# Kernel optimization log

Hardware: AMD Instinct MI355X
Metric: run time of the kernel (lower is better)

The kernel has to match this reference:

```python
import jax, jax.numpy as jnp
import numpy as np
from jax import lax

NUM_QUBITS = 4
NUM_LAYERS = 2
EPS = 1e-5  # BatchNorm eps; eval mode with running_mean=0, running_var=1


def _cnot_ring_matrix():
    # CNOT(0,1); CNOT(1,2); CNOT(2,3); CNOT(3,0) as one 16x16 permutation.
    # PennyLane convention: wire 0 is the most-significant bit of the basis index.
    M = np.zeros((16, 16), dtype=np.complex64)
    for b in range(16):
        bb = b
        for cw, tw in [(0, 1), (1, 2), (2, 3), (3, 0)]:
            if (bb >> (3 - cw)) & 1:
                bb ^= 1 << (3 - tw)
        M[bb, b] = 1.0
    return M

CNOT_RING = jnp.asarray(_cnot_ring_matrix())
# ZSIGNS[w, b] = <b|Z_w|b> = +/-1
ZSIGNS = jnp.asarray(np.array([[1.0 - 2.0 * ((b >> (3 - w)) & 1) for b in range(16)]
                               for w in range(NUM_QUBITS)], dtype=np.float32))


def conv_bn_relu(x, w, b, gamma, beta):
    # Conv2d(k=3, pad=1) + BatchNorm2d (eval: mean=0, var=1) + ReLU, NCHW
    x = lax.conv_general_dilated(x, w, (1, 1), ((1, 1), (1, 1)),
                                 dimension_numbers=('NCHW', 'OIHW', 'NCHW'))
    x = x + b[None, :, None, None]
    x = gamma[None, :, None, None] * x * (1.0 / np.sqrt(1.0 + EPS)) + beta[None, :, None, None]
    return jax.nn.relu(x)


def maxpool2(x):
    return lax.reduce_window(x, -jnp.inf, lax.max, (1, 1, 2, 2), (1, 1, 2, 2), 'VALID')


def avgpool2(x):
    return lax.reduce_window(x, 0.0, lax.add, (1, 1, 2, 2), (1, 1, 2, 2), 'VALID') * 0.25


def quantum_layer(x, weights):
    # x: [B, 16] softmax outputs. Amplitude-encode (abs + L2 normalize), then
    # BasicEntanglerLayers (RX rotations + CNOT ring) x NUM_LAYERS, then <Z_i>.
    psi = jnp.abs(x)
    psi = psi / jnp.linalg.norm(psi, axis=1, keepdims=True)
    psi = psi.astype(jnp.complex64)  # [B, 16] batched statevectors
    for l in range(NUM_LAYERS):
        c = jnp.cos(weights[l] * 0.5).astype(jnp.complex64)
        s = jnp.sin(weights[l] * 0.5).astype(jnp.complex64)
        U = jnp.ones((1, 1), dtype=jnp.complex64)
        for q in range(NUM_QUBITS):
            g = jnp.stack([jnp.stack([c[q], -1j * s[q]]),
                           jnp.stack([-1j * s[q], c[q]])])  # RX(theta_q)
            U = jnp.kron(U, g)
        U = CNOT_RING @ U  # rotations first, then entangling ring
        psi = psi @ U.T    # batched apply: [B,16] x [16,16]
    probs = jnp.real(psi * jnp.conj(psi))  # [B, 16]
    return probs @ ZSIGNS.T                # [B, 4] Pauli-Z expvals


def setup_inputs() -> dict:
    key = jax.random.key(0)
    ks = jax.random.split(key, 16)
    B = 1024
    f32 = jnp.float32

    def w(k, shape, fan_in):
        return jax.random.normal(k, shape, dtype=f32) * np.float32(1.0 / np.sqrt(fan_in))

    inp = {
        'x': jax.random.normal(ks[0], (B, 3, 32, 32), dtype=f32),
        'conv1_w': w(ks[1], (32, 3, 3, 3), 3 * 9), 'conv1_b': jnp.zeros((32,), f32),
        'bn1_g': jnp.ones((32,), f32), 'bn1_b': jnp.zeros((32,), f32),
        'conv2_w': w(ks[2], (64, 32, 3, 3), 32 * 9), 'conv2_b': jnp.zeros((64,), f32),
        'bn2_g': jnp.ones((64,), f32), 'bn2_b': jnp.zeros((64,), f32),
        'conv3_w': w(ks[3], (128, 64, 3, 3), 64 * 9), 'conv3_b': jnp.zeros((128,), f32),
        'bn3_g': jnp.ones((128,), f32), 'bn3_b': jnp.zeros((128,), f32),
        'fr1_w': w(ks[4], (512, 2048), 2048), 'fr1_b': jnp.zeros((512,), f32),
        'fr2_w': w(ks[5], (16, 512), 512), 'fr2_b': jnp.zeros((16,), f32),
        'q_weights': jax.random.uniform(ks[6], (NUM_LAYERS, NUM_QUBITS), dtype=f32,
                                        minval=0.0, maxval=2.0 * np.pi),
        'h1_w': w(ks[7], (128, 4), 4), 'h1_b': jnp.zeros((128,), f32),
        'bnh_g': jnp.ones((128,), f32), 'bnh_b': jnp.zeros((128,), f32),
        'h2_w': w(ks[8], (100, 128), 128), 'h2_b': jnp.zeros((100,), f32),
    }
    return inp


def reference(x, conv1_w, conv1_b, bn1_g, bn1_b, conv2_w, conv2_b, bn2_g, bn2_b,
              conv3_w, conv3_b, bn3_g, bn3_b, fr1_w, fr1_b, fr2_w, fr2_b,
              q_weights, h1_w, h1_b, bnh_g, bnh_b, h2_w, h2_b):
    # classical_net (CIFAR100 branch)
    h = conv_bn_relu(x, conv1_w, conv1_b, bn1_g, bn1_b)
    h = maxpool2(h)                                   # [B,32,16,16]
    h = conv_bn_relu(h, conv2_w, conv2_b, bn2_g, bn2_b)
    h = maxpool2(h)                                   # [B,64,8,8]
    h = conv_bn_relu(h, conv3_w, conv3_b, bn3_g, bn3_b)  # [B,128,8,8]
    h = avgpool2(h)                                   # AdaptiveAvgPool2d((4,4)): 8->4
    h = h.reshape(h.shape[0], -1)                     # [B, 2048]
    # feature_reducer
    h = jax.nn.relu(h @ fr1_w.T + fr1_b)
    f = jax.nn.softmax(h @ fr2_w.T + fr2_b, axis=1)   # [B, 16]
    # quantum layer (batched 4-qubit statevector sim)
    q = quantum_layer(f, q_weights)                   # [B, 4]
    # head (BN eval-mode, Dropout inactive)
    y = q @ h1_w.T + h1_b
    y = bnh_g * y * (1.0 / np.sqrt(1.0 + EPS)) + bnh_b
    y = jax.nn.relu(y)
    return y @ h2_w.T + h2_b                          # [B, 100]
```

## Files before the change

### kernel.cpp

```cpp
#include <hip/hip_runtime.h>
#include <math.h>

#define NB 1024
static constexpr float BN_INV = 0.99999500003749975f;

typedef __attribute__((ext_vector_type(8))) short short8;
typedef __attribute__((ext_vector_type(4))) float f32x4;

__device__ inline short f2bf(float f) {
  union { float f; unsigned u; } v;
  v.f = f;
  unsigned u = v.u;
  u += 0x7fff + ((u >> 16) & 1);
  return (short)(u >> 16);
}

__global__ void k_prepack(const float* __restrict__ c2w, const float* __restrict__ c2b,
                          const float* __restrict__ g2, const float* __restrict__ be2,
                          const float* __restrict__ c3w, const float* __restrict__ c3b,
                          const float* __restrict__ g3, const float* __restrict__ be3,
                          const float* __restrict__ fr1w,
                          short* __restrict__ wp2, short* __restrict__ wp3,
                          float* __restrict__ scsh, short* __restrict__ wfr1) {
  int i = blockIdx.x * 256 + threadIdx.x;
  int stride = gridDim.x * 256;
  for (int e = i; e < 18432; e += stride) {
    int j = e & 7, lane = (e >> 3) & 63, ct = (e >> 9) & 3, off = e >> 11;
    int co = ct * 16 + (lane & 15), ci = (lane >> 4) * 8 + j;
    wp2[e] = f2bf(c2w[(co * 32 + ci) * 9 + off]);
  }
  for (int e = i; e < 73728; e += stride) {
    int j = e & 7, lane = (e >> 3) & 63, ct = (e >> 9) & 7, oh = e >> 12;
    int half = oh & 1, off = oh >> 1;
    int co = ct * 16 + (lane & 15), ci = half * 32 + (lane >> 4) * 8 + j;
    wp3[e] = f2bf(c3w[(co * 64 + ci) * 9 + off]);
  }
  for (int e = i; e < 524288; e += stride) {
    float2 f = ((const float2*)fr1w)[e];
    unsigned lo = (unsigned)(unsigned short)f2bf(f.x);
    unsigned hi = (unsigned)(unsigned short)f2bf(f.y);
    ((unsigned*)wfr1)[e] = (hi << 16) | lo;
  }
  if (i < 64) {
    float sc = g2[i] * BN_INV;
    scsh[i] = sc;
    scsh[64 + i] = sc * c2b[i] + be2[i];
  } else if (i < 192) {
    int c = i - 64;
    float sc = g3[c] * BN_INV;
    scsh[128 + c] = sc;
    scsh[256 + c] = sc * c3b[c] + be3[c];
  }
}

__global__ __launch_bounds__(256) void k_conv1(
    const float* __restrict__ x, const float* __restrict__ w,
    const float* __restrict__ bias, const float* __restrict__ g,
    const float* __restrict__ be, short* __restrict__ out) {
  __shared__ float tile[3 * 34 * 34];
  const int b = blockIdx.x;
  const int tid = threadIdx.x;
  const float* xb = x + b * 3 * 32 * 32;
  for (int i = tid; i < 3 * 34 * 34; i += 256) {
    int c = i / 1156;
    int rem = i - c * 1156;
    int r = rem / 34;
    int col = rem - r * 34;
    int iy = r - 1, ix = col - 1;
    float v = 0.f;
    if (iy >= 0 && iy < 32 && ix >= 0 && ix < 32)
      v = xb[(c * 32 + iy) * 32 + ix];
    tile[i] = v;
  }
  __syncthreads();
  const int tx = tid & 15, ty = tid >> 4;
  float win[3][4][4];
#pragma unroll
  for (int c = 0; c < 3; ++c)
#pragma unroll
    for (int r = 0; r < 4; ++r)
#pragma unroll
      for (int cc = 0; cc < 4; ++cc)
        win[c][r][cc] = tile[c * 1156 + (2 * ty + r) * 34 + 2 * tx + cc];

  for (int co = 0; co < 32; ++co) {
    const float* wp = w + co * 27;
    float a00 = 0.f, a01 = 0.f, a10 = 0.f, a11 = 0.f;
#pragma unroll
    for (int c = 0; c < 3; ++c)
#pragma unroll
      for (int ky = 0; ky < 3; ++ky)
#pragma unroll
        for (int kx = 0; kx < 3; ++kx) {
          float wv = wp[c * 9 + ky * 3 + kx];
          a00 = fmaf(win[c][ky][kx], wv, a00);
          a01 = fmaf(win[c][ky][kx + 1], wv, a01);
          a10 = fmaf(win[c][ky + 1][kx], wv, a10);
          a11 = fmaf(win[c][ky + 1][kx + 1], wv, a11);
        }
    float gg = g[co] * BN_INV, bt = be[co], bs = bias[co];
    float v0 = fmaxf(fmaf(gg, a00 + bs, bt), 0.f);
    float v1 = fmaxf(fmaf(gg, a01 + bs, bt), 0.f);
    float v2 = fmaxf(fmaf(gg, a10 + bs, bt), 0.f);
    float v3 = fmaxf(fmaf(gg, a11 + bs, bt), 0.f);
    float m = fmaxf(fmaxf(v0, v1), fmaxf(v2, v3));
    out[((b * 32 + co) * 16 + ty) * 16 + tx] = f2bf(m);
  }
}

__global__ __launch_bounds__(256) void k_conv2m(
    const short* __restrict__ in ,
    const short* __restrict__ wp2, const float* __restrict__ scsh,
    short* __restrict__ out2 ) {
  __shared__ __align__(16) short inT[18 * 18 * 40];
  const int b = blockIdx.x;
  const int tid = threadIdx.x;
  const int w = tid >> 6, lane = tid & 63, q = lane >> 4, n = lane & 15;

  for (int i = tid; i < 18 * 18 * 40 / 2; i += 256) ((int*)inT)[i] = 0;
  __syncthreads();
  const short* ib = in + (size_t)b * 8192;
  for (int i = tid; i < 8192; i += 256) {
    int ci = i >> 8, y = (i >> 4) & 15, x = i & 15;
    inT[((y + 1) * 18 + (x + 1)) * 40 + ci] = ib[i];
  }
  __syncthreads();

  const short8* wv = (const short8*)wp2;
  f32x4 acc[4][4];
#pragma unroll
  for (int t = 0; t < 4; ++t)
#pragma unroll
    for (int ct = 0; ct < 4; ++ct) acc[t][ct] = (f32x4)0.f;

#pragma unroll
  for (int off = 0; off < 9; ++off) {
    const int ky = off / 3, kx = off % 3;
    short8 a[4];
#pragma unroll
    for (int ct = 0; ct < 4; ++ct) a[ct] = wv[(off * 4 + ct) * 64 + lane];
#pragma unroll
    for (int t = 0; t < 4; ++t) {
      int y = 4 * w + t;
      short8 bf = *(const short8*)&inT[((y + ky) * 18 + (n + kx)) * 40 + q * 8];
#pragma unroll
      for (int ct = 0; ct < 4; ++ct)
        acc[t][ct] =
            __builtin_amdgcn_mfma_f32_16x16x32_bf16(a[ct], bf, acc[t][ct], 0, 0, 0);
    }
  }

  const float* sc2 = scsh;
  const float* sh2 = scsh + 64;
#pragma unroll
  for (int ct = 0; ct < 4; ++ct) {
    float vm[4][4];
#pragma unroll
    for (int t = 0; t < 4; ++t)
#pragma unroll
      for (int r = 0; r < 4; ++r) {
        int co = ct * 16 + q * 4 + r;
        float v = fmaf(sc2[co], acc[t][ct][r], sh2[co]);
        v = fmaxf(v, 0.f);
        vm[t][r] = fmaxf(v, __shfl_xor(v, 1));
      }
#pragma unroll
    for (int pp = 0; pp < 2; ++pp)
#pragma unroll
      for (int r = 0; r < 4; ++r) {
        float m = fmaxf(vm[2 * pp][r], vm[2 * pp + 1][r]);
        if ((n & 1) == 0) {
          int co = ct * 16 + q * 4 + r;
          out2[((size_t)b * 64 + co) * 64 + (2 * w + pp) * 8 + (n >> 1)] = f2bf(m);
        }
      }
  }
}

__global__ __launch_bounds__(256) void k_conv3m(
    const short* __restrict__ in ,
    const short* __restrict__ wp3, const float* __restrict__ scsh,
    short* __restrict__ out3 ) {
  __shared__ __align__(16) short inT3[10 * 10 * 72];
  const int b = blockIdx.x;
  const int tid = threadIdx.x;
  const int w = tid >> 6, lane = tid & 63, q = lane >> 4, n = lane & 15;

  for (int i = tid; i < 10 * 10 * 72 / 2; i += 256) ((int*)inT3)[i] = 0;
  __syncthreads();
  const short* ib = in + (size_t)b * 4096;
  for (int i = tid; i < 4096; i += 256) {
    int ci = i >> 6, y = (i >> 3) & 7, x = i & 7;
    inT3[((y + 1) * 10 + (x + 1)) * 72 + ci] = ib[i];
  }
  __syncthreads();

  const short8* wv = (const short8*)wp3;
  f32x4 acc[4][2];
#pragma unroll
  for (int c = 0; c < 4; ++c)
#pragma unroll
    for (int tt = 0; tt < 2; ++tt) acc[c][tt] = (f32x4)0.f;

  const int ct0 = (w >> 1) * 4;
  const int t0 = (w & 1) * 2;
#pragma unroll
  for (int off = 0; off < 9; ++off) {
    const int ky = off / 3, kx = off % 3;
#pragma unroll
    for (int half = 0; half < 2; ++half) {
      short8 a[4];
#pragma unroll
      for (int c = 0; c < 4; ++c)
        a[c] = wv[((off * 2 + half) * 8 + ct0 + c) * 64 + lane];
#pragma unroll
      for (int tt = 0; tt < 2; ++tt) {
        int y = 2 * (t0 + tt) + (n >> 3), x = n & 7;
        short8 bf = *(const short8*)&inT3[((y + ky) * 10 + (x + kx)) * 72 +
                                          half * 32 + q * 8];
#pragma unroll
        for (int c = 0; c < 4; ++c)
          acc[c][tt] =
              __builtin_amdgcn_mfma_f32_16x16x32_bf16(a[c], bf, acc[c][tt], 0, 0, 0);
      }
    }
  }

  const float* sc3 = scsh + 128;
  const float* sh3 = scsh + 256;
#pragma unroll
  for (int c = 0; c < 4; ++c) {
    int ct = ct0 + c;
#pragma unroll
    for (int tt = 0; tt < 2; ++tt) {
      int t = t0 + tt;
#pragma unroll
      for (int r = 0; r < 4; ++r) {
        int co = ct * 16 + q * 4 + r;
        float v = fmaf(sc3[co], acc[c][tt][r], sh3[co]);
        v = fmaxf(v, 0.f);
        float s = v + __shfl_xor(v, 1);
        s += __shfl_xor(s, 8);
        if ((n & 9) == 0)
          out3[(size_t)b * 2048 + co * 16 + t * 4 + (n >> 1)] = f2bf(s * 0.25f);
      }
    }
  }
}

__global__ __launch_bounds__(256) void k_fr1m(
    const short* __restrict__ A, const short* __restrict__ W,
    const float* __restrict__ bias, float* __restrict__ C) {
  __shared__ __align__(16) short As[32 * 72];
  __shared__ __align__(16) short Bs[32 * 72];
  const int m0 = blockIdx.x * 32;
  const int n0 = blockIdx.y * 32;
  const int tid = threadIdx.x;
  const int w = tid >> 6, lane = tid & 63, q = lane >> 4, n = lane & 15;
  const int mt = w >> 1, nt = w & 1;
  const int srow = tid >> 3, sc = tid & 7;

  f32x4 acc = (f32x4)0.f;
  const short* Ab = A + (size_t)(m0 + srow) * 2048 + sc * 8;
  const short* Wb = W + (size_t)(n0 + srow) * 2048 + sc * 8;

  for (int k0 = 0; k0 < 2048; k0 += 64) {
    short8 av = *(const short8*)(Ab + k0);
    short8 bv = *(const short8*)(Wb + k0);
    __syncthreads();
    *(short8*)&As[srow * 72 + sc * 8] = av;
    *(short8*)&Bs[srow * 72 + sc * 8] = bv;
    __syncthreads();
#pragma unroll
    for (int kk = 0; kk < 2; ++kk) {
      short8 bfrag = *(const short8*)&Bs[(nt * 16 + n) * 72 + kk * 32 + q * 8];
      short8 afrag = *(const short8*)&As[(mt * 16 + n) * 72 + kk * 32 + q * 8];
      acc = __builtin_amdgcn_mfma_f32_16x16x32_bf16(afrag, bfrag, acc, 0, 0, 0);
    }
  }
#pragma unroll
  for (int r = 0; r < 4; ++r) {
    int m = m0 + mt * 16 + q * 4 + r;
    int nn = n0 + nt * 16 + n;
    C[(size_t)m * 512 + nn] = fmaxf(acc[r] + bias[nn], 0.f);
  }
}

__global__ __launch_bounds__(64) void k_tail(
    const float* __restrict__ H, const float* __restrict__ W2,
    const float* __restrict__ b2, const float* __restrict__ qw,
    const float* __restrict__ h1w, const float* __restrict__ h1b,
    const float* __restrict__ bg, const float* __restrict__ bb,
    const float* __restrict__ h2w, const float* __restrict__ h2b,
    float* __restrict__ out) {
  __shared__ float hbuf[512];
  __shared__ float ybuf[128];
  const int b = blockIdx.x;
  const int lane = threadIdx.x;
  const float* hrow = H + b * 512;
  *(float4*)&hbuf[lane * 4] = *(const float4*)&hrow[lane * 4];
  *(float4*)&hbuf[256 + lane * 4] = *(const float4*)&hrow[256 + lane * 4];
  __syncthreads();

  const int j = lane & 15;
  const int grpk = lane >> 4;
  float partial = 0.f;
  const float* wrow = W2 + j * 512 + grpk * 128;
  const float* hb = hbuf + grpk * 128;
#pragma unroll
  for (int k = 0; k < 128; k += 4) {
    float4 wv = *(const float4*)&wrow[k];
    partial = fmaf(wv.x, hb[k + 0], partial);
    partial = fmaf(wv.y, hb[k + 1], partial);
    partial = fmaf(wv.z, hb[k + 2], partial);
    partial = fmaf(wv.w, hb[k + 3], partial);
  }
  partial += __shfl_xor(partial, 16);
  partial += __shfl_xor(partial, 32);
  float logit = partial + b2[j];

  float m = logit;
#pragma unroll
  for (int d = 1; d < 16; d <<= 1) m = fmaxf(m, __shfl_xor(m, d));
  float e = expf(logit - m);
  float s = e;
#pragma unroll
  for (int d = 1; d < 16; d <<= 1) s += __shfl_xor(s, d);
  float p = e / s;

  float n2 = p * p;
#pragma unroll
  for (int d = 1; d < 16; d <<= 1) n2 += __shfl_xor(n2, d);
  float amp = p / sqrtf(n2);
  float re = amp, im = 0.f;

#pragma unroll
  for (int l = 0; l < 2; ++l) {
#pragma unroll
    for (int q = 0; q < 4; ++q) {
      float th = qw[l * 4 + q] * 0.5f;
      float c = cosf(th), sn = sinf(th);
      int mask = 1 << (3 - q);
      float pre = __shfl_xor(re, mask);
      float pim = __shfl_xor(im, mask);
      float nre = fmaf(c, re, sn * pim);
      float nim = fmaf(c, im, -sn * pre);
      re = nre;
      im = nim;
    }
    int src = j;
    if (src & 1) src ^= 8;
    if (src & 2) src ^= 1;
    if (src & 4) src ^= 2;
    if (src & 8) src ^= 4;
    int srclane = (lane & 48) | src;
    re = __shfl(re, srclane);
    im = __shfl(im, srclane);
  }

  float prob = re * re + im * im;
  float qv[4];
#pragma unroll
  for (int w = 0; w < 4; ++w) {
    float sgn = ((j >> (3 - w)) & 1) ? -1.f : 1.f;
    float cwv = prob * sgn;
    cwv += __shfl_xor(cwv, 1);
    cwv += __shfl_xor(cwv, 2);
    cwv += __shfl_xor(cwv, 4);
    cwv += __shfl_xor(cwv, 8);
    qv[w] = cwv;
  }

#pragma unroll
  for (int t = 0; t < 2; ++t) {
    int jj = lane + 64 * t;
    float4 hw = *(const float4*)&h1w[jj * 4];
    float y = h1b[jj];
    y = fmaf(hw.x, qv[0], y);
    y = fmaf(hw.y, qv[1], y);
    y = fmaf(hw.z, qv[2], y);
    y = fmaf(hw.w, qv[3], y);
    y = fmaf(bg[jj] * BN_INV, y, bb[jj]);
    ybuf[jj] = fmaxf(y, 0.f);
  }
  __syncthreads();

#pragma unroll
  for (int t = 0; t < 2; ++t) {
    int k = lane + 64 * t;
    if (k < 100) {
      const float* wr = h2w + k * 128;
      float o = h2b[k];
#pragma unroll
      for (int jj = 0; jj < 128; jj += 4) {
        float4 wv = *(const float4*)&wr[jj];
        o = fmaf(wv.x, ybuf[jj + 0], o);
        o = fmaf(wv.y, ybuf[jj + 1], o);
        o = fmaf(wv.z, ybuf[jj + 2], o);
        o = fmaf(wv.w, ybuf[jj + 3], o);
      }
      out[b * 100 + k] = o;
    }
  }
}

extern "C" void kernel_launch(void* const* d_in, const int* in_sizes, int n_in,
                              void* d_out, int out_size, void* d_ws,
                              size_t ws_size, hipStream_t stream) {
  const float* x = (const float*)d_in[0];
  const float* c1w = (const float*)d_in[1];
  const float* c1b = (const float*)d_in[2];
  const float* g1 = (const float*)d_in[3];
  const float* be1 = (const float*)d_in[4];
  const float* c2w = (const float*)d_in[5];
  const float* c2b = (const float*)d_in[6];
  const float* g2 = (const float*)d_in[7];
  const float* be2 = (const float*)d_in[8];
  const float* c3w = (const float*)d_in[9];
  const float* c3b = (const float*)d_in[10];
  const float* g3 = (const float*)d_in[11];
  const float* be3 = (const float*)d_in[12];
  const float* fr1w = (const float*)d_in[13];
  const float* fr1b = (const float*)d_in[14];
  const float* fr2w = (const float*)d_in[15];
  const float* fr2b = (const float*)d_in[16];
  const float* qwts = (const float*)d_in[17];
  const float* h1w = (const float*)d_in[18];
  const float* h1b = (const float*)d_in[19];
  const float* bhg = (const float*)d_in[20];
  const float* bhb = (const float*)d_in[21];
  const float* h2w = (const float*)d_in[22];
  const float* h2b = (const float*)d_in[23];
  float* out = (float*)d_out;

  float* ws = (float*)d_ws;
  short* out1bf = (short*)ws;
  short* out2bf = (short*)(ws + 4194304);
  short* out3bf = (short*)(ws + 6291456);
  float* h1 = ws + 7340032;
  short* wfr1 = (short*)(ws + 7864320);
  short* wp2 = (short*)(ws + 8388608);
  short* wp3 = (short*)(ws + 8397824);
  float* scsh = ws + 8434688;

  k_prepack<<<96, 256, 0, stream>>>(c2w, c2b, g2, be2, c3w, c3b, g3, be3, fr1w,
                                    wp2, wp3, scsh, wfr1);
  k_conv1<<<NB, 256, 0, stream>>>(x, c1w, c1b, g1, be1, out1bf);
  k_conv2m<<<NB, 256, 0, stream>>>(out1bf, wp2, scsh, out2bf);
  k_conv3m<<<NB, 256, 0, stream>>>(out2bf, wp3, scsh, out3bf);
  k_fr1m<<<dim3(32, 16), 256, 0, stream>>>(out3bf, wfr1, fr1b, h1);
  k_tail<<<NB, 64, 0, stream>>>(h1, fr2w, fr2b, qwts, h1w, h1b, bhg, bhb, h2w,
                                h2b, out);
}
```

Baseline: 199.6 us.

## Fuse conv1/conv2/conv3 into one kernel keeping activations in LDS; batch tail 4 per block

The three conv kernels are merged into one per-image kernel. Conv1's pooled output is written channel-packed straight into the conv2 LDS tile, and conv2's pooled output goes straight into the conv3 LDS tile, so the global-memory round trips for the intermediate activations and two launches are removed. The tail kernel now processes four images per 256-thread block instead of one image per 64-thread block. The fused kernel uses more LDS (about 41 KB per block) and likely more registers, which can lower occupancy.

```diff
diff --git a/kernel.cpp b/kernel.cpp
--- a/kernel.cpp
+++ b/kernel.cpp
@@ -53,14 +53,25 @@
   }
 }
 
-__global__ __launch_bounds__(256) void k_conv1(
-    const float* __restrict__ x, const float* __restrict__ w,
-    const float* __restrict__ bias, const float* __restrict__ g,
-    const float* __restrict__ be, short* __restrict__ out) {
+__global__ __launch_bounds__(256) void k_conv123(
+    const float* __restrict__ x, const float* __restrict__ c1w,
+    const float* __restrict__ c1b, const float* __restrict__ g1,
+    const float* __restrict__ be1, const short* __restrict__ wp2,
+    const short* __restrict__ wp3, const float* __restrict__ scsh,
+    short* __restrict__ out3) {
   __shared__ float tile[3 * 34 * 34];
+  __shared__ __align__(16) short inT[18 * 18 * 40];
+  __shared__ __align__(16) short inT3[10 * 10 * 72];
   const int b = blockIdx.x;
   const int tid = threadIdx.x;
-  const float* xb = x + b * 3 * 32 * 32;
+  const int w = tid >> 6, lane = tid & 63, q = lane >> 4, n = lane & 15;
+
+  {
+    int4 z = {0, 0, 0, 0};
+    for (int i = tid; i < 1620; i += 256) ((int4*)inT)[i] = z;
+    for (int i = tid; i < 900; i += 256) ((int4*)inT3)[i] = z;
+  }
+  const float* xb = x + (size_t)b * 3072;
   for (int i = tid; i < 3 * 34 * 34; i += 256) {
     int c = i / 1156;
     int rem = i - c * 1156;
@@ -73,176 +84,166 @@
     tile[i] = v;
   }
   __syncthreads();
-  const int tx = tid & 15, ty = tid >> 4;
-  float win[3][4][4];
-#pragma unroll
-  for (int c = 0; c < 3; ++c)
-#pragma unroll
-    for (int r = 0; r < 4; ++r)
-#pragma unroll
-      for (int cc = 0; cc < 4; ++cc)
-        win[c][r][cc] = tile[c * 1156 + (2 * ty + r) * 34 + 2 * tx + cc];
-
-  for (int co = 0; co < 32; ++co) {
-    const float* wp = w + co * 27;
-    float a00 = 0.f, a01 = 0.f, a10 = 0.f, a11 = 0.f;
+
+  {
+    const int tx = tid & 15, ty = tid >> 4;
+    float win[3][4][4];
 #pragma unroll
     for (int c = 0; c < 3; ++c)
 #pragma unroll
-      for (int ky = 0; ky < 3; ++ky)
-#pragma unroll
-        for (int kx = 0; kx < 3; ++kx) {
-          float wv = wp[c * 9 + ky * 3 + kx];
-          a00 = fmaf(win[c][ky][kx], wv, a00);
-          a01 = fmaf(win[c][ky][kx + 1], wv, a01);
-          a10 = fmaf(win[c][ky + 1][kx], wv, a10);
-          a11 = fmaf(win[c][ky + 1][kx + 1], wv, a11);
+      for (int r = 0; r < 4; ++r)
+#pragma unroll
+        for (int cc = 0; cc < 4; ++cc)
+          win[c][r][cc] = tile[c * 1156 + (2 * ty + r) * 34 + 2 * tx + cc];
+
+    unsigned pk[16];
+#pragma unroll
+    for (int co = 0; co < 32; ++co) {
+      const float* wp = c1w + co * 27;
+      float a00 = 0.f, a01 = 0.f, a10 = 0.f, a11 = 0.f;
+#pragma unroll
+      for (int c = 0; c < 3; ++c)
+#pragma unroll
+        for (int ky = 0; ky < 3; ++ky)
+#pragma unroll
+          for (int kx = 0; kx < 3; ++kx) {
+            float wv = wp[c * 9 + ky * 3 + kx];
+            a00 = fmaf(win[c][ky][kx], wv, a00);
+            a01 = fmaf(win[c][ky][kx + 1], wv, a01);
+            a10 = fmaf(win[c][ky + 1][kx], wv, a10);
+            a11 = fmaf(win[c][ky + 1][kx + 1], wv, a11);
+          }
+      float gg = g1[co] * BN_INV, bt = be1[co], bs = c1b[co];
+      float v0 = fmaxf(fmaf(gg, a00 + bs, bt), 0.f);
+      float v1 = fmaxf(fmaf(gg, a01 + bs, bt), 0.f);
+      float v2 = fmaxf(fmaf(gg, a10 + bs, bt), 0.f);
+      float v3 = fmaxf(fmaf(gg, a11 + bs, bt), 0.f);
+      float m = fmaxf(fmaxf(v0, v1), fmaxf(v2, v3));
+      unsigned h = (unsigned)(unsigned short)f2bf(m);
+      if (co & 1)
+        pk[co >> 1] |= h << 16;
+      else
+        pk[co >> 1] = h;
+    }
+    short* dst = &inT[((ty + 1) * 18 + (tx + 1)) * 40];
+#pragma unroll
+    for (int i = 0; i < 4; ++i) {
+      int4 v;
+      v.x = (int)pk[4 * i + 0];
+      v.y = (int)pk[4 * i + 1];
+      v.z = (int)pk[4 * i + 2];
+      v.w = (int)pk[4 * i + 3];
+      ((int4*)dst)[i] = v;
+    }
+  }
+  __syncthreads();
+
+  {
+    const short8* wv = (const short8*)wp2;
+    f32x4 acc[4][4];
+#pragma unroll
+    for (int t = 0; t < 4; ++t)
+#pragma unroll
+      for (int ct = 0; ct < 4; ++ct) acc[t][ct] = (f32x4)0.f;
+
+#pragma unroll
+    for (int off = 0; off < 9; ++off) {
+      const int ky = off / 3, kx = off % 3;
+      short8 a[4];
+#pragma unroll
+      for (int ct = 0; ct < 4; ++ct) a[ct] = wv[(off * 4 + ct) * 64 + lane];
+#pragma unroll
+      for (int t = 0; t < 4; ++t) {
+        int y = 4 * w + t;
+        short8 bf = *(const short8*)&inT[((y + ky) * 18 + (n + kx)) * 40 + q * 8];
+#pragma unroll
+        for (int ct = 0; ct < 4; ++ct)
+          acc[t][ct] = __builtin_amdgcn_mfma_f32_16x16x32_bf16(a[ct], bf,
+                                                               acc[t][ct], 0, 0, 0);
+      }
+    }
+
+    const float* sc2 = scsh;
+    const float* sh2 = scsh + 64;
+#pragma unroll
+    for (int ct = 0; ct < 4; ++ct) {
+      float vm[4][4];
+#pragma unroll
+      for (int t = 0; t < 4; ++t)
+#pragma unroll
+        for (int r = 0; r < 4; ++r) {
+          int co = ct * 16 + q * 4 + r;
+          float v = fmaf(sc2[co], acc[t][ct][r], sh2[co]);
+          v = fmaxf(v, 0.f);
+          vm[t][r] = fmaxf(v, __shfl_xor(v, 1));
         }
-    float gg = g[co] * BN_INV, bt = be[co], bs = bias[co];
-    float v0 = fmaxf(fmaf(gg, a00 + bs, bt), 0.f);
-    float v1 = fmaxf(fmaf(gg, a01 + bs, bt), 0.f);
-    float v2 = fmaxf(fmaf(gg, a10 + bs, bt), 0.f);
-    float v3 = fmaxf(fmaf(gg, a11 + bs, bt), 0.f);
-    float m = fmaxf(fmaxf(v0, v1), fmaxf(v2, v3));
-    out[((b * 32 + co) * 16 + ty) * 16 + tx] = f2bf(m);
-  }
-}
-
-__global__ __launch_bounds__(256) void k_conv2m(
-    const short* __restrict__ in ,
-    const short* __restrict__ wp2, const float* __restrict__ scsh,
-    short* __restrict__ out2 ) {
-  __shared__ __align__(16) short inT[18 * 18 * 40];
-  const int b = blockIdx.x;
-  const int tid = threadIdx.x;
-  const int w = tid >> 6, lane = tid & 63, q = lane >> 4, n = lane & 15;
-
-  for (int i = tid; i < 18 * 18 * 40 / 2; i += 256) ((int*)inT)[i] = 0;
-  __syncthreads();
-  const short* ib = in + (size_t)b * 8192;
-  for (int i = tid; i < 8192; i += 256) {
-    int ci = i >> 8, y = (i >> 4) & 15, x = i & 15;
-    inT[((y + 1) * 18 + (x + 1)) * 40 + ci] = ib[i];
-  }
-  __syncthreads();
-
-  const short8* wv = (const short8*)wp2;
-  f32x4 acc[4][4];
-#pragma unroll
-  for (int t = 0; t < 4; ++t)
-#pragma unroll
-    for (int ct = 0; ct < 4; ++ct) acc[t][ct] = (f32x4)0.f;
-
-#pragma unroll
-  for (int off = 0; off < 9; ++off) {
-    const int ky = off / 3, kx = off % 3;
-    short8 a[4];
-#pragma unroll
-    for (int ct = 0; ct < 4; ++ct) a[ct] = wv[(off * 4 + ct) * 64 + lane];
-#pragma unroll
-    for (int t = 0; t < 4; ++t) {
-      int y = 4 * w + t;
-      short8 bf = *(const short8*)&inT[((y + ky) * 18 + (n + kx)) * 40 + q * 8];
-#pragma unroll
-      for (int ct = 0; ct < 4; ++ct)
-        acc[t][ct] =
-            __builtin_amdgcn_mfma_f32_16x16x32_bf16(a[ct], bf, acc[t][ct], 0, 0, 0);
-    }
-  }
-
-  const float* sc2 = scsh;
-  const float* sh2 = scsh + 64;
-#pragma unroll
-  for (int ct = 0; ct < 4; ++ct) {
-    float vm[4][4];
-#pragma unroll
-    for (int t = 0; t < 4; ++t)
-#pragma unroll
-      for (int r = 0; r < 4; ++r) {
-        int co = ct * 16 + q * 4 + r;
-        float v = fmaf(sc2[co], acc[t][ct][r], sh2[co]);
-        v = fmaxf(v, 0.f);
-        vm[t][r] = fmaxf(v, __shfl_xor(v, 1));
-      }
-#pragma unroll
-    for (int pp = 0; pp < 2; ++pp)
-#pragma unroll
-      for (int r = 0; r < 4; ++r) {
-        float m = fmaxf(vm[2 * pp][r], vm[2 * pp + 1][r]);
+#pragma unroll
+      for (int pp = 0; pp < 2; ++pp) {
+        short4 s4;
+#pragma unroll
+        for (int r = 0; r < 4; ++r) {
+          float m = fmaxf(vm[2 * pp][r], vm[2 * pp + 1][r]);
+          ((short*)&s4)[r] = f2bf(m);
+        }
         if ((n & 1) == 0) {
-          int co = ct * 16 + q * 4 + r;
-          out2[((size_t)b * 64 + co) * 64 + (2 * w + pp) * 8 + (n >> 1)] = f2bf(m);
+          int y = 2 * w + pp, xx = n >> 1;
+          *(short4*)&inT3[((y + 1) * 10 + (xx + 1)) * 72 + ct * 16 + q * 4] = s4;
         }
       }
-  }
-}
-
-__global__ __launch_bounds__(256) void k_conv3m(
-    const short* __restrict__ in ,
-    const short* __restrict__ wp3, const float* __restrict__ scsh,
-    short* __restrict__ out3 ) {
-  __shared__ __align__(16) short inT3[10 * 10 * 72];
-  const int b = blockIdx.x;
-  const int tid = threadIdx.x;
-  const int w = tid >> 6, lane = tid & 63, q = lane >> 4, n = lane & 15;
-
-  for (int i = tid; i < 10 * 10 * 72 / 2; i += 256) ((int*)inT3)[i] = 0;
+    }
+  }
   __syncthreads();
-  const short* ib = in + (size_t)b * 4096;
-  for (int i = tid; i < 4096; i += 256) {
-    int ci = i >> 6, y = (i >> 3) & 7, x = i & 7;
-    inT3[((y + 1) * 10 + (x + 1)) * 72 + ci] = ib[i];
-  }
-  __syncthreads();
-
-  const short8* wv = (const short8*)wp3;
-  f32x4 acc[4][2];
-#pragma unroll
-  for (int c = 0; c < 4; ++c)
-#pragma unroll
-    for (int tt = 0; tt < 2; ++tt) acc[c][tt] = (f32x4)0.f;
-
-  const int ct0 = (w >> 1) * 4;
-  const int t0 = (w & 1) * 2;
-#pragma unroll
-  for (int off = 0; off < 9; ++off) {
-    const int ky = off / 3, kx = off % 3;
-#pragma unroll
-    for (int half = 0; half < 2; ++half) {
-      short8 a[4];
-#pragma unroll
-      for (int c = 0; c < 4; ++c)
-        a[c] = wv[((off * 2 + half) * 8 + ct0 + c) * 64 + lane];
+
+  {
+    const short8* wv = (const short8*)wp3;
+    f32x4 acc[4][2];
+#pragma unroll
+    for (int c = 0; c < 4; ++c)
+#pragma unroll
+      for (int tt = 0; tt < 2; ++tt) acc[c][tt] = (f32x4)0.f;
+
+    const int ct0 = (w >> 1) * 4;
+    const int t0 = (w & 1) * 2;
+#pragma unroll
+    for (int off = 0; off < 9; ++off) {
+      const int ky = off / 3, kx = off % 3;
+#pragma unroll
+      for (int half = 0; half < 2; ++half) {
+        short8 a[4];
+#pragma unroll
+        for (int c = 0; c < 4; ++c)
+          a[c] = wv[((off * 2 + half) * 8 + ct0 + c) * 64 + lane];
+#pragma unroll
+        for (int tt = 0; tt < 2; ++tt) {
+          int y = 2 * (t0 + tt) + (n >> 3), xx = n & 7;
+          short8 bf = *(const short8*)&inT3[((y + ky) * 10 + (xx + kx)) * 72 +
+                                            half * 32 + q * 8];
+#pragma unroll
+          for (int c = 0; c < 4; ++c)
+            acc[c][tt] = __builtin_amdgcn_mfma_f32_16x16x32_bf16(a[c], bf,
+                                                                 acc[c][tt], 0, 0, 0);
+        }
+      }
+    }
+
+    const float* sc3 = scsh + 128;
+    const float* sh3 = scsh + 256;
+#pragma unroll
+    for (int c = 0; c < 4; ++c) {
+      int ct = ct0 + c;
 #pragma unroll
       for (int tt = 0; tt < 2; ++tt) {
-        int y = 2 * (t0 + tt) + (n >> 3), x = n & 7;
-        short8 bf = *(const short8*)&inT3[((y + ky) * 10 + (x + kx)) * 72 +
-                                          half * 32 + q * 8];
-#pragma unroll
-        for (int c = 0; c < 4; ++c)
-          acc[c][tt] =
-              __builtin_amdgcn_mfma_f32_16x16x32_bf16(a[c], bf, acc[c][tt], 0, 0, 0);
-      }
-    }
-  }
-
-  const float* sc3 = scsh + 128;
-  const float* sh3 = scsh + 256;
-#pragma unroll
-  for (int c = 0; c < 4; ++c) {
-    int ct = ct0 + c;
-#pragma unroll
-    for (int tt = 0; tt < 2; ++tt) {
-      int t = t0 + tt;
-#pragma unroll
-      for (int r = 0; r < 4; ++r) {
-        int co = ct * 16 + q * 4 + r;
-        float v = fmaf(sc3[co], acc[c][tt][r], sh3[co]);
-        v = fmaxf(v, 0.f);
-        float s = v + __shfl_xor(v, 1);
-        s += __shfl_xor(s, 8);
-        if ((n & 9) == 0)
-          out3[(size_t)b * 2048 + co * 16 + t * 4 + (n >> 1)] = f2bf(s * 0.25f);
+        int t = t0 + tt;
+#pragma unroll
+        for (int r = 0; r < 4; ++r) {
+          int co = ct * 16 + q * 4 + r;
+          float v = fmaf(sc3[co], acc[c][tt][r], sh3[co]);
+          v = fmaxf(v, 0.f);
+          float s = v + __shfl_xor(v, 1);
+          s += __shfl_xor(s, 8);
+          if ((n & 9) == 0)
+            out3[(size_t)b * 2048 + co * 16 + t * 4 + (n >> 1)] = f2bf(s * 0.25f);
+        }
       }
     }
   }
@@ -286,34 +287,35 @@
   }
 }
 
-__global__ __launch_bounds__(64) void k_tail(
+__global__ __launch_bounds__(256) void k_tail4(
     const float* __restrict__ H, const float* __restrict__ W2,
     const float* __restrict__ b2, const float* __restrict__ qw,
     const float* __restrict__ h1w, const float* __restrict__ h1b,
     const float* __restrict__ bg, const float* __restrict__ bb,
     const float* __restrict__ h2w, const float* __restrict__ h2b,
     float* __restrict__ out) {
-  __shared__ float hbuf[512];
-  __shared__ float ybuf[128];
-  const int b = blockIdx.x;
-  const int lane = threadIdx.x;
-  const float* hrow = H + b * 512;
-  *(float4*)&hbuf[lane * 4] = *(const float4*)&hrow[lane * 4];
-  *(float4*)&hbuf[256 + lane * 4] = *(const float4*)&hrow[256 + lane * 4];
+  __shared__ float hbuf[4][512];
+  __shared__ float ybuf[4][128];
+  const int wv4 = threadIdx.x >> 6;
+  const int lane = threadIdx.x & 63;
+  const int b = blockIdx.x * 4 + wv4;
+  const float* hrow = H + (size_t)b * 512;
+  *(float4*)&hbuf[wv4][lane * 4] = *(const float4*)&hrow[lane * 4];
+  *(float4*)&hbuf[wv4][256 + lane * 4] = *(const float4*)&hrow[256 + lane * 4];
   __syncthreads();
 
   const int j = lane & 15;
   const int grpk = lane >> 4;
   float partial = 0.f;
   const float* wrow = W2 + j * 512 + grpk * 128;
-  const float* hb = hbuf + grpk * 128;
+  const float* hb = hbuf[wv4] + grpk * 128;
 #pragma unroll
   for (int k = 0; k < 128; k += 4) {
-    float4 wv = *(const float4*)&wrow[k];
-    partial = fmaf(wv.x, hb[k + 0], partial);
-    partial = fmaf(wv.y, hb[k + 1], partial);
-    partial = fmaf(wv.z, hb[k + 2], partial);
-    partial = fmaf(wv.w, hb[k + 3], partial);
+    float4 wvv = *(const float4*)&wrow[k];
+    partial = fmaf(wvv.x, hb[k + 0], partial);
+    partial = fmaf(wvv.y, hb[k + 1], partial);
+    partial = fmaf(wvv.z, hb[k + 2], partial);
+    partial = fmaf(wvv.w, hb[k + 3], partial);
   }
   partial += __shfl_xor(partial, 16);
   partial += __shfl_xor(partial, 32);
@@ -381,7 +383,7 @@
     y = fmaf(hw.z, qv[2], y);
     y = fmaf(hw.w, qv[3], y);
     y = fmaf(bg[jj] * BN_INV, y, bb[jj]);
-    ybuf[jj] = fmaxf(y, 0.f);
+    ybuf[wv4][jj] = fmaxf(y, 0.f);
   }
   __syncthreads();
 
@@ -391,15 +393,16 @@
     if (k < 100) {
       const float* wr = h2w + k * 128;
       float o = h2b[k];
+      const float* yb = ybuf[wv4];
 #pragma unroll
       for (int jj = 0; jj < 128; jj += 4) {
-        float4 wv = *(const float4*)&wr[jj];
-        o = fmaf(wv.x, ybuf[jj + 0], o);
-        o = fmaf(wv.y, ybuf[jj + 1], o);
-        o = fmaf(wv.z, ybuf[jj + 2], o);
-        o = fmaf(wv.w, ybuf[jj + 3], o);
+        float4 wvv = *(const float4*)&wr[jj];
+        o = fmaf(wvv.x, yb[jj + 0], o);
+        o = fmaf(wvv.y, yb[jj + 1], o);
+        o = fmaf(wvv.z, yb[jj + 2], o);
+        o = fmaf(wvv.w, yb[jj + 3], o);
       }
-      out[b * 100 + k] = o;
+      out[(size_t)b * 100 + k] = o;
     }
   }
 }
@@ -434,21 +437,18 @@
   float* out = (float*)d_out;
 
   float* ws = (float*)d_ws;
-  short* out1bf = (short*)ws;
-  short* out2bf = (short*)(ws + 4194304);
-  short* out3bf = (short*)(ws + 6291456);
-  float* h1 = ws + 7340032;
-  short* wfr1 = (short*)(ws + 7864320);
-  short* wp2 = (short*)(ws + 8388608);
-  short* wp3 = (short*)(ws + 8397824);
-  float* scsh = ws + 8434688;
+  short* out3bf = (short*)ws;
+  float* h1 = ws + 1048576;
+  short* wfr1 = (short*)(ws + 1572864);
+  short* wp2 = (short*)(ws + 2097152);
+  short* wp3 = (short*)(ws + 2106368);
+  float* scsh = ws + 2143232;
 
   k_prepack<<<96, 256, 0, stream>>>(c2w, c2b, g2, be2, c3w, c3b, g3, be3, fr1w,
                                     wp2, wp3, scsh, wfr1);
-  k_conv1<<<NB, 256, 0, stream>>>(x, c1w, c1b, g1, be1, out1bf);
-  k_conv2m<<<NB, 256, 0, stream>>>(out1bf, wp2, scsh, out2bf);
-  k_conv3m<<<NB, 256, 0, stream>>>(out2bf, wp3, scsh, out3bf);
+  k_conv123<<<NB, 256, 0, stream>>>(x, c1w, c1b, g1, be1, wp2, wp3, scsh,
+                                    out3bf);
   k_fr1m<<<dim3(32, 16), 256, 0, stream>>>(out3bf, wfr1, fr1b, h1);
-  k_tail<<<NB, 64, 0, stream>>>(h1, fr2w, fr2b, qwts, h1w, h1b, bhg, bhb, h2w,
-                                h2b, out);
-}
+  k_tail4<<<256, 256, 0, stream>>>(h1, fr2w, fr2b, qwts, h1w, h1b, bhg, bhb,
+                                   h2w, h2b, out);
+}
```

New measurement: 213.8 us. +7.1%, slower.

## Replace LDS-tiled fr1 GEMM with per-wave direct-load MFMA and pack tail blocks

Applied to the files above, without the earlier changes.

The feature-reducer GEMM no longer stages tiles through shared memory with two barriers per K step. Each wave now computes one 16x16 output tile, loading its MFMA fragments straight from global memory and writing a float4 per lane, which removes the synchronisation. The price is that operand reuse across waves in a block is lost and global reads become strided. The tail kernel now processes four samples per 256-thread block instead of one per 64-thread block, cutting the block count.

```diff
diff --git a/kernel.cpp b/kernel.cpp
--- a/kernel.cpp
+++ b/kernel.cpp
@@ -248,72 +248,61 @@
   }
 }
 
-__global__ __launch_bounds__(256) void k_fr1m(
-    const short* __restrict__ A, const short* __restrict__ W,
-    const float* __restrict__ bias, float* __restrict__ C) {
-  __shared__ __align__(16) short As[32 * 72];
-  __shared__ __align__(16) short Bs[32 * 72];
-  const int m0 = blockIdx.x * 32;
-  const int n0 = blockIdx.y * 32;
-  const int tid = threadIdx.x;
-  const int w = tid >> 6, lane = tid & 63, q = lane >> 4, n = lane & 15;
-  const int mt = w >> 1, nt = w & 1;
-  const int srow = tid >> 3, sc = tid & 7;
-
+__global__ __launch_bounds__(256) void k_fr1w(
+    const short* __restrict__ out3, const short* __restrict__ wfr1,
+    const float* __restrict__ bias, float* __restrict__ h1) {
+  const int gw = blockIdx.x * 4 + (threadIdx.x >> 6);
+  const int lane = threadIdx.x & 63, q = lane >> 4, n = lane & 15;
+  const int mt = gw & 31, nt = gw >> 5;
+  const short* Ap = wfr1 + (size_t)(mt * 16 + n) * 2048 + q * 8;
+  const short* Bp = out3 + (size_t)(nt * 16 + n) * 2048 + q * 8;
   f32x4 acc = (f32x4)0.f;
-  const short* Ab = A + (size_t)(m0 + srow) * 2048 + sc * 8;
-  const short* Wb = W + (size_t)(n0 + srow) * 2048 + sc * 8;
-
-  for (int k0 = 0; k0 < 2048; k0 += 64) {
-    short8 av = *(const short8*)(Ab + k0);
-    short8 bv = *(const short8*)(Wb + k0);
-    __syncthreads();
-    *(short8*)&As[srow * 72 + sc * 8] = av;
-    *(short8*)&Bs[srow * 72 + sc * 8] = bv;
-    __syncthreads();
-#pragma unroll
-    for (int kk = 0; kk < 2; ++kk) {
-      short8 bfrag = *(const short8*)&Bs[(nt * 16 + n) * 72 + kk * 32 + q * 8];
-      short8 afrag = *(const short8*)&As[(mt * 16 + n) * 72 + kk * 32 + q * 8];
-      acc = __builtin_amdgcn_mfma_f32_16x16x32_bf16(afrag, bfrag, acc, 0, 0, 0);
-    }
-  }
-#pragma unroll
-  for (int r = 0; r < 4; ++r) {
-    int m = m0 + mt * 16 + q * 4 + r;
-    int nn = n0 + nt * 16 + n;
-    C[(size_t)m * 512 + nn] = fmaxf(acc[r] + bias[nn], 0.f);
-  }
-}
-
-__global__ __launch_bounds__(64) void k_tail(
+#pragma unroll 8
+  for (int k0 = 0; k0 < 2048; k0 += 32) {
+    short8 av = *(const short8*)(Ap + k0);
+    short8 bv = *(const short8*)(Bp + k0);
+    acc = __builtin_amdgcn_mfma_f32_16x16x32_bf16(av, bv, acc, 0, 0, 0);
+  }
+  const int sample = nt * 16 + n;
+  const int hid0 = mt * 16 + q * 4;
+  float4 bi = *(const float4*)&bias[hid0];
+  float4 o;
+  o.x = fmaxf(acc[0] + bi.x, 0.f);
+  o.y = fmaxf(acc[1] + bi.y, 0.f);
+  o.z = fmaxf(acc[2] + bi.z, 0.f);
+  o.w = fmaxf(acc[3] + bi.w, 0.f);
+  *(float4*)&h1[(size_t)sample * 512 + hid0] = o;
+}
+
+__global__ __launch_bounds__(256) void k_tail4(
     const float* __restrict__ H, const float* __restrict__ W2,
     const float* __restrict__ b2, const float* __restrict__ qw,
     const float* __restrict__ h1w, const float* __restrict__ h1b,
     const float* __restrict__ bg, const float* __restrict__ bb,
     const float* __restrict__ h2w, const float* __restrict__ h2b,
     float* __restrict__ out) {
-  __shared__ float hbuf[512];
-  __shared__ float ybuf[128];
-  const int b = blockIdx.x;
-  const int lane = threadIdx.x;
-  const float* hrow = H + b * 512;
-  *(float4*)&hbuf[lane * 4] = *(const float4*)&hrow[lane * 4];
-  *(float4*)&hbuf[256 + lane * 4] = *(const float4*)&hrow[256 + lane * 4];
+  __shared__ float hbuf[4][512];
+  __shared__ float ybuf[4][128];
+  const int wv4 = threadIdx.x >> 6;
+  const int lane = threadIdx.x & 63;
+  const int b = blockIdx.x * 4 + wv4;
+  const float* hrow = H + (size_t)b * 512;
+  *(float4*)&hbuf[wv4][lane * 4] = *(const float4*)&hrow[lane * 4];
+  *(float4*)&hbuf[wv4][256 + lane * 4] = *(const float4*)&hrow[256 + lane * 4];
   __syncthreads();
 
   const int j = lane & 15;
   const int grpk = lane >> 4;
   float partial = 0.f;
   const float* wrow = W2 + j * 512 + grpk * 128;
-  const float* hb = hbuf + grpk * 128;
+  const float* hb = hbuf[wv4] + grpk * 128;
 #pragma unroll
   for (int k = 0; k < 128; k += 4) {
-    float4 wv = *(const float4*)&wrow[k];
-    partial = fmaf(wv.x, hb[k + 0], partial);
-    partial = fmaf(wv.y, hb[k + 1], partial);
-    partial = fmaf(wv.z, hb[k + 2], partial);
-    partial = fmaf(wv.w, hb[k + 3], partial);
+    float4 wvv = *(const float4*)&wrow[k];
+    partial = fmaf(wvv.x, hb[k + 0], partial);
+    partial = fmaf(wvv.y, hb[k + 1], partial);
+    partial = fmaf(wvv.z, hb[k + 2], partial);
+    partial = fmaf(wvv.w, hb[k + 3], partial);
   }
   partial += __shfl_xor(partial, 16);
   partial += __shfl_xor(partial, 32);
@@ -381,7 +370,7 @@
     y = fmaf(hw.z, qv[2], y);
     y = fmaf(hw.w, qv[3], y);
     y = fmaf(bg[jj] * BN_INV, y, bb[jj]);
-    ybuf[jj] = fmaxf(y, 0.f);
+    ybuf[wv4][jj] = fmaxf(y, 0.f);
   }
   __syncthreads();
 
@@ -391,15 +380,16 @@
     if (k < 100) {
       const float* wr = h2w + k * 128;
       float o = h2b[k];
+      const float* yb = ybuf[wv4];
 #pragma unroll
       for (int jj = 0; jj < 128; jj += 4) {
-        float4 wv = *(const float4*)&wr[jj];
-        o = fmaf(wv.x, ybuf[jj + 0], o);
-        o = fmaf(wv.y, ybuf[jj + 1], o);
-        o = fmaf(wv.z, ybuf[jj + 2], o);
-        o = fmaf(wv.w, ybuf[jj + 3], o);
+        float4 wvv = *(const float4*)&wr[jj];
+        o = fmaf(wvv.x, yb[jj + 0], o);
+        o = fmaf(wvv.y, yb[jj + 1], o);
+        o = fmaf(wvv.z, yb[jj + 2], o);
+        o = fmaf(wvv.w, yb[jj + 3], o);
       }
-      out[b * 100 + k] = o;
+      out[(size_t)b * 100 + k] = o;
     }
   }
 }
@@ -448,7 +438,7 @@
   k_conv1<<<NB, 256, 0, stream>>>(x, c1w, c1b, g1, be1, out1bf);
   k_conv2m<<<NB, 256, 0, stream>>>(out1bf, wp2, scsh, out2bf);
   k_conv3m<<<NB, 256, 0, stream>>>(out2bf, wp3, scsh, out3bf);
-  k_fr1m<<<dim3(32, 16), 256, 0, stream>>>(out3bf, wfr1, fr1b, h1);
-  k_tail<<<NB, 64, 0, stream>>>(h1, fr2w, fr2b, qwts, h1w, h1b, bhg, bhb, h2w,
-                                h2b, out);
-}
+  k_fr1w<<<512, 256, 0, stream>>>(out3bf, wfr1, fr1b, h1);
+  k_tail4<<<256, 256, 0, stream>>>(h1, fr2w, fr2b, qwts, h1w, h1b, bhg, bhb,
+                                   h2w, h2b, out);
+}
```

Result: slower. 217.0 us (+8.7%).
